# Kernel tuning notes

Measured on AMD Instinct MI355X. Metric: run time of the kernel, lower is better.

Reference implementation:

```python
import jax, jax.numpy as jnp
import numpy as np
import math

SCALE = 16.0
IGNORE_THRES = 0.5
BAD_CONF_WEIGHT = 1.25
NB, NT, NA, NH, NW, NC = 16, 50, 5, 128, 128, 20


def _inv_tanh(y):
    ys = jnp.clip(y, -1.0 + 1e-6, 1.0 - 1e-6)
    at = 0.5 * jnp.log((1.0 + ys) / (1.0 - ys))
    return jnp.where(y <= -1.0, -2.0, jnp.where(y >= 1.0, 2.0, at))


def _forward(prediction, target, target_sizes, anchors):
    nB, nA, nH, nW, _ = prediction.shape
    nC = prediction.shape[-1] - 6
    s = SCALE
    # scaled anchors and anchor corner points (matches __init__ precompute)
    aw = anchors[:, 0] / s
    ah = anchors[:, 1] / s
    ar = anchors[:, 2]
    cr, sr = jnp.cos(ar), jnp.sin(ar)
    anchor_points = jnp.stack([-cr * aw, sr * aw, cr * aw, -sr * aw,
                               -sr * ah, -cr * ah, sr * ah, cr * ah], axis=1)  # [nA,8]
    anchor_hws = (ah + aw) / 2.0

    pred_conf = prediction[..., 0]
    x = prediction[..., 1]; y = prediction[..., 2]; r = prediction[..., 3]
    h = prediction[..., 4]; w = prediction[..., 5]
    pred_cls = prediction[..., 6:]

    # ---- build_targets_dist, vectorized (original uses detached .cpu().data) ----
    tgt = jax.lax.stop_gradient(target)
    T = tgt.shape[1]
    valid = jnp.arange(T)[None, :] < target_sizes[:, None]
    gx = tgt[..., 0] / s; gy = tgt[..., 1] / s
    gw = tgt[..., 4] / s; gh = tgt[..., 3] / s
    gr = tgt[..., 2]
    valid = valid & (gw != 0) & (gh != 0)
    gi = jnp.clip(gx.astype(jnp.int32), 0, nW - 1)
    gj = jnp.clip(gy.astype(jnp.int32), 0, nH - 1)
    pts = tgt[..., 5:13] / s
    cpts = pts - jnp.tile(jnp.stack([gx, gy], axis=-1), (1, 1, 4))  # centered corners [nB,T,8]
    deltas = cpts[:, :, None, :] - anchor_points[None, None, :, :]  # [nB,T,nA,8]
    dn = sum(jnp.linalg.norm(deltas[..., i:i + 2], axis=-1) for i in (0, 2, 4, 6))
    norm = (((gh + gw) / 2.0)[:, :, None] + anchor_hws[None, None, :]) / 2.0
    anch_dists = (dn / norm) ** 2  # [nB,T,nA]

    # conf_mask: zero anchors closer than ignore_thres at (gj,gi)
    conf_mask = jnp.ones((nB, nA, nH, nW), jnp.float32)
    b3 = jnp.broadcast_to(jnp.arange(nB)[:, None, None], (nB, T, nA)).reshape(-1)
    a3 = jnp.broadcast_to(jnp.arange(nA)[None, None, :], (nB, T, nA)).reshape(-1)
    gj3 = jnp.broadcast_to(gj[:, :, None], (nB, T, nA)).reshape(-1)
    gi3 = jnp.broadcast_to(gi[:, :, None], (nB, T, nA)).reshape(-1)
    ign = ((anch_dists < IGNORE_THRES) & valid[:, :, None]).reshape(-1)
    conf_mask = conf_mask.at[b3, a3, gj3, gi3].min(jnp.where(ign, 0.0, 1.0))

    best_n = jnp.argmin(anch_dists, axis=-1)  # [nB,T]
    txv = _inv_tanh(gx - (gi.astype(jnp.float32) + 0.5))
    tyv = _inv_tanh(gy - (gj.astype(jnp.float32) + 0.5))
    rd = gr - ar[best_n]
    rd = jnp.where(rd > math.pi, rd - 2 * math.pi,
                   jnp.where(rd < -math.pi, rd + 2 * math.pi, rd))
    trv = _inv_tanh(rd / (math.pi / 2))
    twv = jnp.log(gw / aw[best_n] + 1e-16)
    thv = jnp.log(gh / ah[best_n] + 1e-16)
    tlabv = jnp.argmax(tgt[..., 13:], axis=-1)

    bS = jnp.where(valid, jnp.arange(nB)[:, None], -1).reshape(-1)  # -1 -> dropped
    idx = (bS, best_n.reshape(-1), gj.reshape(-1), gi.reshape(-1))
    z = jnp.zeros((nB, nA, nH, nW), jnp.float32)
    mask = z.at[idx].set(1.0, mode='drop')
    conf_mask = conf_mask.at[idx].set(1.0, mode='drop')
    tx = z.at[idx].set(txv.reshape(-1), mode='drop')
    ty = z.at[idx].set(tyv.reshape(-1), mode='drop')
    tw = z.at[idx].set(twv.reshape(-1), mode='drop')
    th = z.at[idx].set(thv.reshape(-1), mode='drop')
    tr = z.at[idx].set(trv.reshape(-1), mode='drop')
    tconf = mask  # tconf set to 1 exactly where mask is 1
    tlab = jnp.zeros((nB, nA, nH, nW), jnp.int32).at[idx].set(
        tlabv.reshape(-1).astype(jnp.int32), mode='drop')

    conf_mask_false = conf_mask * (1.0 - mask)

    def masked_bce(z_, t_, m_):
        l = jnp.maximum(z_, 0.0) - z_ * t_ + jnp.log1p(jnp.exp(-jnp.abs(z_)))
        return jnp.sum(l * m_) / jnp.maximum(jnp.sum(m_), 1.0)

    def masked_mse(p_, t_):
        return jnp.sum(((p_ - t_) ** 2) * mask) / jnp.maximum(jnp.sum(mask), 1.0)

    loss_conf = BAD_CONF_WEIGHT * masked_bce(pred_conf, tconf, conf_mask_false) \
        + masked_bce(pred_conf, tconf, mask)
    loss_x = masked_mse(x, tx); loss_y = masked_mse(y, ty)
    loss_w = masked_mse(w, tw); loss_h = masked_mse(h, th)
    loss_r = masked_mse(r, tr)
    logp = jax.nn.log_softmax(pred_cls, axis=-1)
    nll = -jnp.take_along_axis(logp, tlab[..., None], axis=-1)[..., 0]
    loss_cls = jnp.sum(nll * mask) / jnp.maximum(jnp.sum(mask), 1.0)
    return loss_x + loss_y + loss_w + loss_h + loss_r + loss_conf + loss_cls


def setup_inputs():
    key = jax.random.key(0)
    ks = jax.random.split(key, 8)
    s = SCALE
    prediction = jax.random.normal(ks[0], (NB, NA, NH, NW, 6 + NC), jnp.float32) * 0.5
    # targets in image pixel space (grid is NHxNW at stride SCALE)
    cx = jax.random.uniform(ks[1], (NB, NT), minval=1.0, maxval=NW - 1.0) * s
    cy = jax.random.uniform(ks[2], (NB, NT), minval=1.0, maxval=NH - 1.0) * s
    bw = jax.random.uniform(ks[3], (NB, NT), minval=8.0, maxval=96.0)
    bh = jax.random.uniform(ks[4], (NB, NT), minval=8.0, maxval=48.0)
    br = jax.random.uniform(ks[5], (NB, NT), minval=-0.3, maxval=0.3)
    c, si = jnp.cos(br), jnp.sin(br)
    pts = jnp.stack([cx - c * bw, cy + si * bw, cx + c * bw, cy - si * bw,
                     cx - si * bh, cy - c * bh, cx + si * bh, cy + c * bh], axis=-1)
    cls = jax.nn.one_hot(jax.random.randint(ks[6], (NB, NT), 0, NC), NC, dtype=jnp.float32)
    target = jnp.concatenate([jnp.stack([cx, cy, br, bh, bw], axis=-1), pts, cls], axis=-1)
    target_sizes = jax.random.randint(ks[7], (NB,), 20, NT + 1).astype(jnp.int32)
    anchors = jnp.array([[48., 16., 0.], [96., 24., 0.], [192., 32., 0.],
                         [64., 64., 0.], [32., 96., 1.5708]], jnp.float32)
    return {"prediction": prediction, "target": target,
            "target_sizes": target_sizes, "anchors": anchors}


def reference(prediction, target, target_sizes, anchors):
    return _forward(prediction, target, target_sizes, anchors)
```

## Files before the change

kernel.cpp:

```cpp
#include <hip/hip_runtime.h>
#include <math.h>

#define NBb 16
#define NTt 50
#define NAa 5
#define NHh 128
#define NWw 128
#define NCc 20
#define NCH 26
#define NCELL (NBb*NAa*NHh*NWw)
#define NREC  (NBb*NTt)
#define NSLOT 6
#define NLIST (NREC*NSLOT)
#define SCALE_F 16.0f
#define IGNORE_THRES_F 0.5f
#define BAD_CONF_WEIGHT_F 1.25f
#define PI_F 3.14159265358979323846f

#define NCOPY 16
#define ACC_OFF 16
#define REC_OFF 272
#define LIST_OFF 5072
#define STATUS_OFF 16384

#define MARK_IGN 0x7FFFFFFFu
#define MARK_MASK_BASE 0x3FFFFFFFu
#define CLAIMED 0xFFFFFFFFu

__device__ __forceinline__ bool is_mark(unsigned u) {
  return (u >= (MARK_MASK_BASE - (NREC - 1)) && u <= MARK_MASK_BASE) || (u == MARK_IGN);
}

__device__ __forceinline__ void mark_cell(unsigned* addr, unsigned val) {
  unsigned cur = *addr;
  while (true) {
    unsigned desired = is_mark(cur) ? (cur < val ? cur : val) : val;
    if (desired == cur) break;
    unsigned old = atomicCAS(addr, cur, desired);
    if (old == cur) break;
    cur = old;
  }
}

__device__ __forceinline__ float inv_tanh_f(float y) {
  if (y <= -1.0f) return -2.0f;
  if (y >= 1.0f)  return  2.0f;
  float ys = fminf(fmaxf(y, -1.0f + 1e-6f), 1.0f - 1e-6f);
  return 0.5f * logf((1.0f + ys) / (1.0f - ys));
}

__device__ __forceinline__ float softplus_f(float z) {
  return fmaxf(z, 0.0f) + log1pf(expf(-fabsf(z)));
}

__global__ void k_prep(const float* __restrict__ tgt,
                       const int* __restrict__ tsz,
                       const float* __restrict__ anch,
                       float* __restrict__ ws) {
  int tid = blockIdx.x * blockDim.x + threadIdx.x;
  unsigned* wsu = (unsigned*)ws;
  if (tid < ACC_OFF + NCOPY*16) wsu[tid] = 0u;
  if (tid >= NREC) return;

  unsigned* list = wsu + LIST_OFF;
  #pragma unroll
  for (int s = 0; s < NSLOT; ++s) list[tid*NSLOT + s] = CLAIMED;

  int b = tid / NTt, t = tid % NTt;

  float aw[NAa], ah[NAa], ar[NAa], ahw[NAa], ap[NAa][8];
  for (int a = 0; a < NAa; ++a) {
    aw[a] = anch[a*3+0] / SCALE_F;
    ah[a] = anch[a*3+1] / SCALE_F;
    ar[a] = anch[a*3+2];
    float cr = cosf(ar[a]), sr = sinf(ar[a]);
    ap[a][0] = -cr*aw[a]; ap[a][1] =  sr*aw[a];
    ap[a][2] =  cr*aw[a]; ap[a][3] = -sr*aw[a];
    ap[a][4] = -sr*ah[a]; ap[a][5] = -cr*ah[a];
    ap[a][6] =  sr*ah[a]; ap[a][7] =  cr*ah[a];
    ahw[a] = (ah[a] + aw[a]) * 0.5f;
  }

  const float* row = tgt + (size_t)tid * (13 + NCc);
  float gx = row[0] / SCALE_F;
  float gy = row[1] / SCALE_F;
  float gr = row[2];
  float gh = row[3] / SCALE_F;
  float gw = row[4] / SCALE_F;
  bool valid = (t < tsz[b]) && (gw != 0.0f) && (gh != 0.0f);
  if (!valid) return;

  int gi = (int)gx; gi = min(max(gi, 0), NWw - 1);
  int gj = (int)gy; gj = min(max(gj, 0), NHh - 1);

  float cp[8];
  for (int k = 0; k < 8; ++k)
    cp[k] = row[5 + k] / SCALE_F - ((k & 1) ? gy : gx);

  float bestd = 1e30f; int best = 0; unsigned ignm = 0;
  for (int a = 0; a < NAa; ++a) {
    float dn = 0.0f;
    for (int p = 0; p < 8; p += 2) {
      float dx = cp[p]   - ap[a][p];
      float dy = cp[p+1] - ap[a][p+1];
      dn += sqrtf(dx*dx + dy*dy);
    }
    float nm = ((gh + gw) * 0.5f + ahw[a]) * 0.5f;
    float d = dn / nm; d = d * d;
    if (d < IGNORE_THRES_F) ignm |= (1u << a);
    if (d < bestd) { bestd = d; best = a; }
  }

  unsigned* status = wsu + STATUS_OFF;
  int cellbase = ((b * NAa) * NHh + gj) * NWw + gi;
  int nslot = 0;
  for (int a = 0; a < NAa; ++a)
    if ((ignm >> a) & 1u) {
      int cell = cellbase + a * NHh * NWw;
      mark_cell(&status[cell], MARK_IGN);
      list[tid*NSLOT + nslot++] = (unsigned)cell;
    }
  {
    int cell = cellbase + best * NHh * NWw;
    mark_cell(&status[cell], MARK_MASK_BASE - (unsigned)tid);
    if (!((ignm >> best) & 1u))
      list[tid*NSLOT + nslot++] = (unsigned)cell;
  }

  float txv = inv_tanh_f(gx - ((float)gi + 0.5f));
  float tyv = inv_tanh_f(gy - ((float)gj + 0.5f));
  float rd = gr - ar[best];
  if (rd > PI_F) rd -= 2.0f * PI_F;
  else if (rd < -PI_F) rd += 2.0f * PI_F;
  float trv = inv_tanh_f(rd / (PI_F * 0.5f));
  float twv = logf(gw / aw[best] + 1e-16f);
  float thv = logf(gh / ah[best] + 1e-16f);
  int tlab = 0; float bm = row[13];
  for (int c = 1; c < NCc; ++c)
    if (row[13 + c] > bm) { bm = row[13 + c]; tlab = c; }

  float* rec = ws + REC_OFF;
  rec[0*NREC + tid] = txv;
  rec[1*NREC + tid] = tyv;
  rec[2*NREC + tid] = twv;
  rec[3*NREC + tid] = thv;
  rec[4*NREC + tid] = trv;
  ((int*)rec)[5*NREC + tid] = tlab;
}

#define MAIN_GRID 1024
#define MAIN_BLK  256
#define MAIN_STRIDE (MAIN_GRID*MAIN_BLK)
static_assert(NCELL == 5 * MAIN_STRIDE, "conf loop unroll assumes 5 cells/thread");

__global__ void __launch_bounds__(MAIN_BLK) k_main(const float* __restrict__ pred,
                                                   float* __restrict__ ws) {
  unsigned* wsu = (unsigned*)ws;
  unsigned* status = wsu + STATUS_OFF;
  const unsigned* list = wsu + LIST_OFF;
  const float* rec = ws + REC_OFF;
  int t = blockIdx.x * MAIN_BLK + threadIdx.x;

  float acc = 0.0f;
  #pragma unroll
  for (int k = 0; k < 5; ++k) {
    float z = pred[(size_t)(t + k * MAIN_STRIDE) * NCH];
    acc += softplus_f(z);
  }

  float sub = 0.0f, cnb = 0.0f, obj = 0.0f;
  float sx = 0.0f, sy = 0.0f, sw = 0.0f, sh = 0.0f, sr = 0.0f;
  float scls = 0.0f, cm = 0.0f;

  if (t < NLIST) {
    unsigned cell = list[t];
    if (cell < (unsigned)NCELL) {
      unsigned st = atomicExch(&status[cell], CLAIMED);
      if (is_mark(st)) {
        const float* cpt = pred + (size_t)cell * NCH;
        float z = cpt[0];
        sub = softplus_f(z);
        cnb = 1.0f;
        if (st != MARK_IGN) {
          int r = (int)(MARK_MASK_BASE - st);
          obj = softplus_f(z) - z;
          float dx = cpt[1] - rec[0*NREC + r];
          float dy = cpt[2] - rec[1*NREC + r];
          float dr = cpt[3] - rec[4*NREC + r];
          float dh = cpt[4] - rec[3*NREC + r];
          float dw = cpt[5] - rec[2*NREC + r];
          sx = dx*dx; sy = dy*dy; sw = dw*dw; sh = dh*dh; sr = dr*dr;
          int tlab = ((const int*)rec)[5*NREC + r];
          float m = cpt[6];
          for (int c = 1; c < NCc; ++c) m = fmaxf(m, cpt[6 + c]);
          float s = 0.0f;
          for (int c = 0; c < NCc; ++c) s += expf(cpt[6 + c] - m);
          scls = (m + logf(s)) - cpt[6 + tlab];
          cm = 1.0f;
        }
      }
    }
  }

  float vals[11] = {acc, sub, cnb, obj, sx, sy, sw, sh, sr, scls, cm};
  __shared__ float red[4][11];
  int wid = threadIdx.x >> 6, lane = threadIdx.x & 63;
  #pragma unroll
  for (int k = 0; k < 11; ++k) {
    float v = vals[k];
    for (int off = 32; off; off >>= 1) v += __shfl_down(v, off, 64);
    if (lane == 0) red[wid][k] = v;
  }
  __syncthreads();
  int copy = blockIdx.x & (NCOPY - 1);
  if (threadIdx.x < 11) {
    float v = red[0][threadIdx.x] + red[1][threadIdx.x]
            + red[2][threadIdx.x] + red[3][threadIdx.x];
    if (v != 0.0f) atomicAdd(&ws[ACC_OFF + copy*16 + threadIdx.x], v);
  }
}

__global__ void k_fin(const float* __restrict__ ws, float* __restrict__ out) {
  __shared__ float tot[11];
  if (threadIdx.x < 11) {
    float v = 0.0f;
    for (int c = 0; c < NCOPY; ++c) v += ws[ACC_OFF + c*16 + threadIdx.x];
    tot[threadIdx.x] = v;
  }
  __syncthreads();
  if (threadIdx.x == 0) {
    float acc_bg = tot[0] - tot[1];
    float cnt_bg = (float)NCELL - tot[2];
    float db = fmaxf(cnt_bg, 1.0f);
    float dm = fmaxf(tot[10], 1.0f);
    float loss_conf = BAD_CONF_WEIGHT_F * (acc_bg / db) + tot[3] / dm;
    out[0] = (tot[4] + tot[5] + tot[6] + tot[7] + tot[8] + tot[9]) / dm + loss_conf;
  }
}

extern "C" void kernel_launch(void* const* d_in, const int* in_sizes, int n_in,
                              void* d_out, int out_size, void* d_ws, size_t ws_size,
                              hipStream_t stream) {
  const float* pred = (const float*)d_in[0];
  const float* tgt  = (const float*)d_in[1];
  const int*   tsz  = (const int*)d_in[2];
  const float* anch = (const float*)d_in[3];
  float* ws = (float*)d_ws;

  k_prep<<<4, 256, 0, stream>>>(tgt, tsz, anch, ws);
  k_main<<<MAIN_GRID, MAIN_BLK, 0, stream>>>(pred, ws);
  k_fin<<<1, 64, 0, stream>>>(ws, (float*)d_out);
}
```

Baseline: 213.7 us.

## Stream prediction tensor with coalesced float4 loads and pick out conf channels

Replaces the strided scalar reads of the conf channel (one float every 26) with fully coalesced float4 reads over the whole prediction tensor. Each block covers a 512-cell tile, and each thread keeps the two conf values that fall in its 13 float4 loads, selected by modular index arithmetic. This turns scattered, poorly coalesced loads into contiguous streaming. The cost is reading every channel explicitly and using a larger grid.

Measured after the change: 209.9 us. Within noise of the previous version (-1.8%).

```diff
diff --git a/kernel.cpp b/kernel.cpp
--- a/kernel.cpp
+++ b/kernel.cpp
@@ -9,6 +9,8 @@
 #define NCc 20
 #define NCH 26
 #define NCELL (NBb*NAa*NHh*NWw)
+#define NFLAT (NCELL*NCH)
+#define NQ4   (NFLAT/4)
 #define NREC  (NBb*NTt)
 #define NSLOT 6
 #define NLIST (NREC*NSLOT)
@@ -148,25 +150,32 @@
   ((int*)rec)[5*NREC + tid] = tlab;
 }
 
-#define MAIN_GRID 1024
 #define MAIN_BLK  256
-#define MAIN_STRIDE (MAIN_GRID*MAIN_BLK)
-static_assert(NCELL == 5 * MAIN_STRIDE, "conf loop unroll assumes 5 cells/thread");
-
-__global__ void __launch_bounds__(MAIN_BLK) k_main(const float* __restrict__ pred,
+#define TILE_Q4   (MAIN_BLK*13)
+#define MAIN_GRID (NQ4 / TILE_Q4)
+static_assert(MAIN_GRID * TILE_Q4 == NQ4, "tile decomposition must be exact");
+
+__global__ void __launch_bounds__(MAIN_BLK) k_main(const float4* __restrict__ pred4,
                                                    float* __restrict__ ws) {
   unsigned* wsu = (unsigned*)ws;
   unsigned* status = wsu + STATUS_OFF;
   const unsigned* list = wsu + LIST_OFF;
   const float* rec = ws + REC_OFF;
+  const float* pred = (const float*)pred4;
   int t = blockIdx.x * MAIN_BLK + threadIdx.x;
 
-  float acc = 0.0f;
+  int r = threadIdx.x % 13;
+  int k1 = (39 - 3*r) % 13;
+  int k2 = (57 - 3*r) % 13;
+  const float4* base = pred4 + (size_t)blockIdx.x * TILE_Q4 + threadIdx.x;
+  float cx = 0.0f, cz = 0.0f;
   #pragma unroll
-  for (int k = 0; k < 5; ++k) {
-    float z = pred[(size_t)(t + k * MAIN_STRIDE) * NCH];
-    acc += softplus_f(z);
-  }
+  for (int k = 0; k < 13; ++k) {
+    float4 v = base[k * MAIN_BLK];
+    cx = (k == k1) ? v.x : cx;
+    cz = (k == k2) ? v.z : cz;
+  }
+  float acc = softplus_f(cx) + softplus_f(cz);
 
   float sub = 0.0f, cnb = 0.0f, obj = 0.0f;
   float sx = 0.0f, sy = 0.0f, sw = 0.0f, sh = 0.0f, sr = 0.0f;
@@ -182,15 +191,15 @@
         sub = softplus_f(z);
         cnb = 1.0f;
         if (st != MARK_IGN) {
-          int r = (int)(MARK_MASK_BASE - st);
+          int rr = (int)(MARK_MASK_BASE - st);
           obj = softplus_f(z) - z;
-          float dx = cpt[1] - rec[0*NREC + r];
-          float dy = cpt[2] - rec[1*NREC + r];
-          float dr = cpt[3] - rec[4*NREC + r];
-          float dh = cpt[4] - rec[3*NREC + r];
-          float dw = cpt[5] - rec[2*NREC + r];
+          float dx = cpt[1] - rec[0*NREC + rr];
+          float dy = cpt[2] - rec[1*NREC + rr];
+          float dr = cpt[3] - rec[4*NREC + rr];
+          float dh = cpt[4] - rec[3*NREC + rr];
+          float dw = cpt[5] - rec[2*NREC + rr];
           sx = dx*dx; sy = dy*dy; sw = dw*dw; sh = dh*dh; sr = dr*dr;
-          int tlab = ((const int*)rec)[5*NREC + r];
+          int tlab = ((const int*)rec)[5*NREC + rr];
           float m = cpt[6];
           for (int c = 1; c < NCc; ++c) m = fmaxf(m, cpt[6 + c]);
           float s = 0.0f;
@@ -248,6 +257,6 @@
   float* ws = (float*)d_ws;
 
   k_prep<<<4, 256, 0, stream>>>(tgt, tsz, anch, ws);
-  k_main<<<MAIN_GRID, MAIN_BLK, 0, stream>>>(pred, ws);
+  k_main<<<MAIN_GRID, MAIN_BLK, 0, stream>>>((const float4*)pred, ws);
   k_fin<<<1, 64, 0, stream>>>(ws, (float*)d_out);
 }
```
